# Optimization experiments

Hardware: AMD Instinct MI355X
Metric: run time of the kernel (lower is better)

The kernel has to match this reference:

```python
import jax, jax.numpy as jnp
import numpy as np

N = 1_000_000   # total cluster nodes
D = 128         # input_dim
B = 4096        # number of scenes (segments)
M = 1024        # rows in dist embeddings


def setup_inputs() -> dict:
    key = jax.random.key(0)
    ks = jax.random.split(key, 16)
    inp = {
        "x_clu": jax.random.normal(ks[0], (N, D), dtype=jnp.float32),
        "mask_clu": jax.random.bernoulli(ks[1], 0.9, (N,)),
        "batch_clu": jnp.sort(jax.random.randint(ks[2], (N,), 0, B, dtype=jnp.int32)),
        "dist_embedding": jax.random.normal(ks[3], (M, 6), dtype=jnp.float32),
        "dist_embedding_norm": jax.random.normal(ks[4], (M, 1), dtype=jnp.float32),
        # AttentionalAggregation gate: Linear(D, 1)
        "gate_w": jax.random.normal(ks[5], (D, 1), dtype=jnp.float32) / np.sqrt(D),
        "gate_b": jnp.zeros((1,), dtype=jnp.float32),
        # vel_si_vec MLP [D, D, 6]
        "w1": jax.random.normal(ks[6], (D, D), dtype=jnp.float32) / np.sqrt(D),
        "b1": jnp.zeros((D,), dtype=jnp.float32),
        "w2": jax.random.normal(ks[7], (D, 6), dtype=jnp.float32) / np.sqrt(D),
        "b2": jnp.zeros((6,), dtype=jnp.float32),
        # vel_si_norm MLP [D, D, 1]
        "w1n": jax.random.normal(ks[8], (D, D), dtype=jnp.float32) / np.sqrt(D),
        "b1n": jnp.zeros((D,), dtype=jnp.float32),
        "w2n": jax.random.normal(ks[9], (D, 1), dtype=jnp.float32) / np.sqrt(D),
        "b2n": jnp.zeros((1,), dtype=jnp.float32),
    }
    return inp


def _attn_pool(x, mask, seg, gate_w, gate_b):
    # gate logits for every node; masked nodes excluded from the segment softmax
    gate = jnp.einsum("nd,do->n", x, gate_w) + gate_b[0]           # [N]
    neg = jnp.finfo(gate.dtype).min
    gate = jnp.where(mask, gate, neg)
    gmax = jax.ops.segment_max(gate, seg, num_segments=B)          # [B]
    e = jnp.where(mask, jnp.exp(gate - gmax[seg]), 0.0)            # [N]
    denom = jax.ops.segment_sum(e, seg, num_segments=B)            # [B]
    w = e / jnp.maximum(denom[seg], 1e-12)                         # [N]
    return jax.ops.segment_sum(w[:, None] * x, seg, num_segments=B)  # [B, D]


def reference(x_clu, mask_clu, batch_clu, dist_embedding, dist_embedding_norm,
              gate_w, gate_b, w1, b1, w2, b2, w1n, b1n, w2n, b2n):
    x_scene = _attn_pool(x_clu, mask_clu, batch_clu, gate_w, gate_b)  # [B, D]
    vel = jax.nn.relu(x_scene @ w1 + b1) @ w2 + b2                    # [B, 6]
    nrm = jax.nn.relu(x_scene @ w1n + b1n) @ w2n + b2n                # [B, 1]
    out_vec = vel * jnp.mean(dist_embedding, axis=0)                  # [B, 6]
    out_norm = nrm * jnp.mean(dist_embedding_norm, axis=0)            # [B, 1]
    return out_vec, out_norm
```

## Files before the change

kernel.cpp:

```cpp
#include <hip/hip_runtime.h>

#define D 128

__global__ void means_kernel(const float* __restrict__ de, const float* __restrict__ den,
                             int M, float* __restrict__ out7) {
    __shared__ float sm[256][8];
    float a[7];
#pragma unroll
    for (int j = 0; j < 7; ++j) a[j] = 0.f;
    for (int r = threadIdx.x; r < M; r += 256) {
#pragma unroll
        for (int j = 0; j < 6; ++j) a[j] += de[r * 6 + j];
        a[6] += den[r];
    }
#pragma unroll
    for (int j = 0; j < 7; ++j) sm[threadIdx.x][j] = a[j];
    __syncthreads();
    for (int s = 128; s > 0; s >>= 1) {
        if (threadIdx.x < (unsigned)s) {
#pragma unroll
            for (int j = 0; j < 7; ++j) sm[threadIdx.x][j] += sm[threadIdx.x + s][j];
        }
        __syncthreads();
    }
    if (threadIdx.x < 7) out7[threadIdx.x] = sm[0][threadIdx.x] / (float)M;
}

__global__ void pool_mlp_kernel(const float* __restrict__ x, const int* __restrict__ mask,
                                const int* __restrict__ seg, int N,
                                const float* __restrict__ gate_w, const float* __restrict__ gate_b,
                                const float* __restrict__ w1, const float* __restrict__ b1,
                                const float* __restrict__ w2, const float* __restrict__ b2,
                                const float* __restrict__ w1n, const float* __restrict__ b1n,
                                const float* __restrict__ w2n, const float* __restrict__ b2n,
                                const float* __restrict__ means,
                                float* __restrict__ out_vec, float* __restrict__ out_norm) {
    const int b    = blockIdx.x;
    const int tid  = threadIdx.x;
    const int wv   = tid >> 6;
    const int lane = tid & 63;
    const int half = lane >> 5;
    const int l32  = lane & 31;
    const int hw   = (wv << 1) | half;

    int lo = 0, hi = N;
    while (lo < hi) { int mid = (lo + hi) >> 1; if (seg[mid] < b) lo = mid + 1; else hi = mid; }
    const int start = lo;
    hi = N;
    while (lo < hi) { int mid = (lo + hi) >> 1; if (seg[mid] < b + 1) lo = mid + 1; else hi = mid; }
    const int end = lo;

    const float4 gw4 = ((const float4*)gate_w)[l32];
    const float  gb  = gate_b[0];

    float  s = 0.f;
    float4 acc = {0.f, 0.f, 0.f, 0.f};

    for (int i = start; i < end; i += 8) {
        const int row = i + (hw & 6) + half;
        const bool valid = (row < end) && (mask[row] != 0);
        float4 xv = {0.f, 0.f, 0.f, 0.f};
        if (valid) xv = *(const float4*)(x + (size_t)row * D + l32 * 4);
        float p = xv.x * gw4.x + xv.y * gw4.y + xv.z * gw4.z + xv.w * gw4.w;
#pragma unroll
        for (int off = 16; off > 0; off >>= 1) p += __shfl_xor(p, off);
        const float e = valid ? __expf(p + gb) : 0.f;
        s     += e;
        acc.x += e * xv.x;
        acc.y += e * xv.y;
        acc.z += e * xv.z;
        acc.w += e * xv.w;
    }

    __shared__ float sacc[8][D];
    __shared__ float ss[8];
    *(float4*)&sacc[hw][l32 * 4] = acc;
    if (l32 == 0) ss[hw] = s;
    __syncthreads();

    __shared__ float xs[D];
    if (tid < D) {
        float S = 0.f, A = 0.f;
#pragma unroll
        for (int h = 0; h < 8; ++h) { S += ss[h]; A += sacc[h][tid]; }
        xs[tid] = A / fmaxf(S, 1e-12f);
    }
    __syncthreads();

    __shared__ float hid[D], hidn[D];
    if (tid < D) {
        float a1 = b1[tid];
#pragma unroll 8
        for (int i = 0; i < D; ++i) a1 += xs[i] * w1[i * D + tid];
        hid[tid] = fmaxf(a1, 0.f);
    } else {
        const int h = tid - D;
        float a1n = b1n[h];
#pragma unroll 8
        for (int i = 0; i < D; ++i) a1n += xs[i] * w1n[i * D + h];
        hidn[h] = fmaxf(a1n, 0.f);
    }
    __syncthreads();

    if (tid < 6) {
        float o = b2[tid];
#pragma unroll 8
        for (int i = 0; i < D; ++i) o += hid[i] * w2[i * 6 + tid];
        out_vec[b * 6 + tid] = o * means[tid];
    }
    if (tid == 64) {
        float o = b2n[0];
#pragma unroll 8
        for (int i = 0; i < D; ++i) o += hidn[i] * w2n[i];
        out_norm[b] = o * means[6];
    }
}

extern "C" void kernel_launch(void* const* d_in, const int* in_sizes, int n_in,
                              void* d_out, int out_size, void* d_ws, size_t ws_size,
                              hipStream_t stream) {
    const float* x      = (const float*)d_in[0];
    const int*   mask   = (const int*)  d_in[1];
    const int*   seg    = (const int*)  d_in[2];
    const float* de     = (const float*)d_in[3];
    const float* den    = (const float*)d_in[4];
    const float* gate_w = (const float*)d_in[5];
    const float* gate_b = (const float*)d_in[6];
    const float* w1     = (const float*)d_in[7];
    const float* b1     = (const float*)d_in[8];
    const float* w2     = (const float*)d_in[9];
    const float* b2     = (const float*)d_in[10];
    const float* w1n    = (const float*)d_in[11];
    const float* b1n    = (const float*)d_in[12];
    const float* w2n    = (const float*)d_in[13];
    const float* b2n    = (const float*)d_in[14];

    const int N  = in_sizes[1];
    const int M  = in_sizes[4];
    const int Bn = out_size / 7;

    float* means    = (float*)d_ws;
    float* out_vec  = (float*)d_out;
    float* out_norm = (float*)d_out + (size_t)Bn * 6;

    means_kernel<<<1, 256, 0, stream>>>(de, den, M, means);
    pool_mlp_kernel<<<Bn, 256, 0, stream>>>(x, mask, seg, N, gate_w, gate_b,
                                            w1, b1, w2, b2, w1n, b1n, w2n, b2n,
                                            means, out_vec, out_norm);
}
```

Before: 719.8 us.

## Precompute segment offsets and widen per-wave row processing in pooling kernel

Adds a kernel that scans the sorted segment ids once and writes segment start offsets, replacing two binary searches per block over the full id array. The pooling loop now handles 16 rows per iteration, with 16 lanes per row each loading two float4s, and is unrolled by two. Out-of-range rows are clamped to the last valid row instead of branching, and the mask is applied after the load. The final 128-to-7 projection is split across 112 threads with a shuffle reduction instead of 7 serial threads. The cost is one extra launch and some redundant loads of the clamped tail rows.

```diff
diff --git a/kernel.cpp b/kernel.cpp
--- a/kernel.cpp
+++ b/kernel.cpp
@@ -26,8 +26,17 @@
     if (threadIdx.x < 7) out7[threadIdx.x] = sm[0][threadIdx.x] / (float)M;
 }
 
+__global__ void bounds_kernel(const int* __restrict__ seg, int N, int B,
+                              int* __restrict__ off) {
+    int i = blockIdx.x * blockDim.x + threadIdx.x;
+    if (i > N) return;
+    int cur  = (i < N) ? seg[i]     : B;
+    int prev = (i > 0) ? seg[i - 1] : -1;
+    for (int j = prev + 1; j <= cur; ++j) off[j] = i;
+}
+
 __global__ void pool_mlp_kernel(const float* __restrict__ x, const int* __restrict__ mask,
-                                const int* __restrict__ seg, int N,
+                                const int* __restrict__ off,
                                 const float* __restrict__ gate_w, const float* __restrict__ gate_b,
                                 const float* __restrict__ w1, const float* __restrict__ b1,
                                 const float* __restrict__ w2, const float* __restrict__ b2,
@@ -39,50 +48,52 @@
     const int tid  = threadIdx.x;
     const int wv   = tid >> 6;
     const int lane = tid & 63;
-    const int half = lane >> 5;
-    const int l32  = lane & 31;
-    const int hw   = (wv << 1) | half;
+    const int q    = lane >> 4;
+    const int l16  = lane & 15;
+    const int part = (wv << 2) | q;
 
-    int lo = 0, hi = N;
-    while (lo < hi) { int mid = (lo + hi) >> 1; if (seg[mid] < b) lo = mid + 1; else hi = mid; }
-    const int start = lo;
-    hi = N;
-    while (lo < hi) { int mid = (lo + hi) >> 1; if (seg[mid] < b + 1) lo = mid + 1; else hi = mid; }
-    const int end = lo;
+    const int start = off[b];
+    const int end   = off[b + 1];
 
-    const float4 gw4 = ((const float4*)gate_w)[l32];
+    const float4 gwA = ((const float4*)gate_w)[l16];
+    const float4 gwB = ((const float4*)gate_w)[16 + l16];
     const float  gb  = gate_b[0];
 
-    float  s = 0.f;
-    float4 acc = {0.f, 0.f, 0.f, 0.f};
+    float  s    = 0.f;
+    float4 accA = {0.f, 0.f, 0.f, 0.f};
+    float4 accB = {0.f, 0.f, 0.f, 0.f};
 
-    for (int i = start; i < end; i += 8) {
-        const int row = i + (hw & 6) + half;
-        const bool valid = (row < end) && (mask[row] != 0);
-        float4 xv = {0.f, 0.f, 0.f, 0.f};
-        if (valid) xv = *(const float4*)(x + (size_t)row * D + l32 * 4);
-        float p = xv.x * gw4.x + xv.y * gw4.y + xv.z * gw4.z + xv.w * gw4.w;
+    const int last = end - 1;
+#pragma unroll 2
+    for (int i = start; i < end; i += 16) {
+        const int row = i + (wv << 2) + q;
+        const int r   = min(row, last);
+        const float* xr = x + (size_t)r * D;
+        const float4 xa = ((const float4*)xr)[l16];
+        const float4 xb = ((const float4*)xr)[16 + l16];
+        const int    mk = mask[r];
+        float p = xa.x * gwA.x + xa.y * gwA.y + xa.z * gwA.z + xa.w * gwA.w
+                + xb.x * gwB.x + xb.y * gwB.y + xb.z * gwB.z + xb.w * gwB.w;
 #pragma unroll
-        for (int off = 16; off > 0; off >>= 1) p += __shfl_xor(p, off);
-        const float e = valid ? __expf(p + gb) : 0.f;
+        for (int o = 8; o > 0; o >>= 1) p += __shfl_xor(p, o);
+        const float e = (row < end && mk != 0) ? __expf(p + gb) : 0.f;
         s     += e;
-        acc.x += e * xv.x;
-        acc.y += e * xv.y;
-        acc.z += e * xv.z;
-        acc.w += e * xv.w;
+        accA.x += e * xa.x; accA.y += e * xa.y; accA.z += e * xa.z; accA.w += e * xa.w;
+        accB.x += e * xb.x; accB.y += e * xb.y; accB.z += e * xb.z; accB.w += e * xb.w;
     }
 
-    __shared__ float sacc[8][D];
-    __shared__ float ss[8];
-    *(float4*)&sacc[hw][l32 * 4] = acc;
-    if (l32 == 0) ss[hw] = s;
+    __shared__ float sacc[16][D + 4];
+    __shared__ float ss[16];
+    *(float4*)&sacc[part][l16 * 4]      = accA;
+    *(float4*)&sacc[part][64 + l16 * 4] = accB;
+    if (l16 == 0) ss[part] = s;
     __syncthreads();
 
     __shared__ float xs[D];
     if (tid < D) {
         float S = 0.f, A = 0.f;
 #pragma unroll
-        for (int h = 0; h < 8; ++h) { S += ss[h]; A += sacc[h][tid]; }
+        for (int h = 0; h < 16; ++h) { S += ss[h]; A += sacc[h][tid]; }
         xs[tid] = A / fmaxf(S, 1e-12f);
     }
     __syncthreads();
@@ -102,17 +113,22 @@
     }
     __syncthreads();
 
-    if (tid < 6) {
-        float o = b2[tid];
-#pragma unroll 8
-        for (int i = 0; i < D; ++i) o += hid[i] * w2[i * 6 + tid];
-        out_vec[b * 6 + tid] = o * means[tid];
-    }
-    if (tid == 64) {
-        float o = b2n[0];
-#pragma unroll 8
-        for (int i = 0; i < D; ++i) o += hidn[i] * w2n[i];
-        out_norm[b] = o * means[6];
+    if (tid < 112) {
+        const int g = tid >> 4, l = tid & 15;
+        float o = 0.f;
+        if (g < 6) {
+#pragma unroll
+            for (int k = 0; k < 8; ++k) { const int i = l * 8 + k; o += hid[i] * w2[i * 6 + g]; }
+        } else {
+#pragma unroll
+            for (int k = 0; k < 8; ++k) { const int i = l * 8 + k; o += hidn[i] * w2n[i]; }
+        }
+#pragma unroll
+        for (int of = 8; of > 0; of >>= 1) o += __shfl_xor(o, of);
+        if (l == 0) {
+            if (g < 6) out_vec[b * 6 + g] = (o + b2[g]) * means[g];
+            else       out_norm[b]        = (o + b2n[0]) * means[6];
+        }
     }
 }
 
@@ -140,11 +156,13 @@
     const int Bn = out_size / 7;
 
     float* means    = (float*)d_ws;
+    int*   off      = (int*)d_ws + 16;
     float* out_vec  = (float*)d_out;
     float* out_norm = (float*)d_out + (size_t)Bn * 6;
 
     means_kernel<<<1, 256, 0, stream>>>(de, den, M, means);
-    pool_mlp_kernel<<<Bn, 256, 0, stream>>>(x, mask, seg, N, gate_w, gate_b,
+    bounds_kernel<<<(N + 256) / 256, 256, 0, stream>>>(seg, N, Bn, off);
+    pool_mlp_kernel<<<Bn, 256, 0, stream>>>(x, mask, off, gate_w, gate_b,
                                             w1, b1, w2, b2, w1n, b1n, w2n, b2n,
                                             means, out_vec, out_norm);
 }
```

New measurement: 693.9 us. -3.6%, faster.
